# Kernel optimization log

Hardware: AMD Instinct MI355X
Metric: run time of the kernel (lower is better)

The kernel has to match this reference:

```python
import jax, jax.numpy as jnp
import numpy as np

FILTER_SIZE = 4      # pooled output size (wH = wW = 4)
STRIDE = 16          # feature stride -> spatial_scale = 1/16
C = 512              # feature_dim
H = W = 22           # feature map size (352px crop / stride 16)
NI, NS = 3, 64       # images_in_sequence, sequences
KCELLS = 6           # static bound on integer cells overlapped per bin per axis


def setup_inputs() -> dict:
    key = jax.random.key(0)
    k1, k2, k3, k4 = jax.random.split(key, 4)
    feat = jax.random.normal(k1, (NI, NS, C, H, W), dtype=jnp.float32)
    # bb = (x, y, w, h) in image coords; keep boxes inside 352px image
    xy = jax.random.uniform(k2, (NI, NS, 2), minval=0.0, maxval=96.0)
    wh = jax.random.uniform(k3, (NI, NS, 2), minval=64.0, maxval=224.0)
    bb = jnp.concatenate([xy, wh], axis=-1).astype(jnp.float32)
    # conv init: normal(0, sqrt(2/(k*k*out_ch))), zero bias (as in the torch module)
    std = np.float32(np.sqrt(2.0 / (3 * 3 * C)))
    conv_w = jax.random.normal(k4, (C, C, 3, 3), dtype=jnp.float32) * std
    conv_b = jnp.zeros((C,), jnp.float32)
    return {"feat": feat, "bb": bb, "conv_w": conv_w, "conv_b": conv_b}


def _axis_weights(start, end, size):
    """Exact PrRoIPool 1D integration weights on integer grid points.
    start, end: (N, P) continuous bin boundaries in feature coords.
    Returns (N, P, size) weights s.t. integral of the piecewise-linear
    interpolant over [start, end] = sum_i w[i] * f(i)."""
    N, P = start.shape
    s0 = jnp.floor(start).astype(jnp.int32)                  # first cell
    cell = s0[..., None] + jnp.arange(KCELLS, dtype=jnp.int32)  # (N,P,K)
    cf = cell.astype(start.dtype)
    a1 = jnp.maximum(start[..., None], cf)                   # cell-bin intersection
    a2 = jnp.maximum(jnp.minimum(end[..., None], cf + 1.0), a1)
    alpha = a1 - cf
    lim = a2 - cf
    # integral of (1-t) and t over [alpha, lim]  (PrRoIPoolingMatCalculation)
    f0 = (lim - 0.5 * lim * lim) - (alpha - 0.5 * alpha * alpha)  # weight at point `cell`
    f1 = 0.5 * lim * lim - 0.5 * alpha * alpha                    # weight at `cell+1`
    idx0, idx1 = cell, cell + 1
    v0 = (idx0 >= 0) & (idx0 < size)   # out-of-bounds feature reads are 0
    v1 = (idx1 >= 0) & (idx1 < size)
    wts = jnp.concatenate([jnp.where(v0, f0, 0.0), jnp.where(v1, f1, 0.0)], -1)
    idx = jnp.concatenate([jnp.clip(idx0, 0, size - 1), jnp.clip(idx1, 0, size - 1)], -1)
    out = jnp.zeros((N, P, size), start.dtype)
    n_i = jnp.arange(N)[:, None, None]
    p_i = jnp.arange(P)[None, :, None]
    return out.at[n_i, p_i, idx].add(wts)


def prroi_pool(feat, rois, pooled, scale):
    """Precise RoI pooling. feat: (N,C,H,W); rois: (N,4) = (x1,y1,x2,y2),
    image coords; roi i pools from image i. Returns (N,C,pooled,pooled)."""
    x1, y1, x2, y2 = (rois[:, k] * scale for k in range(4))
    bin_w = (x2 - x1) / pooled
    bin_h = (y2 - y1) / pooled
    p = jnp.arange(pooled, dtype=feat.dtype)
    sh = y1[:, None] + p * bin_h[:, None]; eh = sh + bin_h[:, None]   # (N,P)
    sw = x1[:, None] + p * bin_w[:, None]; ew = sw + bin_w[:, None]
    Wy = _axis_weights(sh, eh, feat.shape[2])   # (N,P,H)
    Wx = _axis_weights(sw, ew, feat.shape[3])   # (N,P,W)
    acc = jnp.einsum('nph,nqw,nchw->ncpq', Wy, Wx, feat)
    area = jnp.maximum(bin_h * bin_w, 0.0)[:, None, None, None]
    return jnp.where(area == 0, 0.0, acc / jnp.where(area == 0, 1.0, area))


def reference(feat, bb, conv_w, conv_b):
    ni = feat.shape[0]
    x = feat.reshape(-1, C, H, W)
    x = jax.lax.conv_general_dilated(
        x, conv_w, window_strides=(1, 1), padding=((1, 1), (1, 1)),
        dimension_numbers=('NCHW', 'OIHW', 'NCHW')) + conv_b[None, :, None, None]
    b = bb.reshape(-1, 4)
    rois = jnp.concatenate([b[:, :2], b[:, :2] + b[:, 2:]], axis=-1)  # xyxy
    w = prroi_pool(x, rois, FILTER_SIZE, 1.0 / STRIDE)
    w = w.reshape(ni, -1, C, FILTER_SIZE, FILTER_SIZE).mean(axis=0)   # mean over images
    return w / (C * FILTER_SIZE * FILTER_SIZE)                        # filter_norm
```

## Files before the change

kernel.cpp:

```cpp
#include <hip/hip_runtime.h>


#define NIMG 192
#define CCH 512
#define FH 22
#define FW 22
#define SPATIAL 484
#define KDIM 4608
#define NDIM 1024
#define KQ 8
#define KSEG 576
#define CISTRIDE 1968
#define POOLBLKS 2048

typedef __bf16 bf16;
typedef __bf16 bf16x2 __attribute__((ext_vector_type(2)));
typedef __bf16 bf16x8 __attribute__((ext_vector_type(8)));
typedef float f32x2 __attribute__((ext_vector_type(2)));
typedef float f32x4 __attribute__((ext_vector_type(4)));

#define GLOBAL_AS __attribute__((address_space(1)))
#define LDS_AS __attribute__((address_space(3)))

__device__ __forceinline__ void gload_lds16(const void* g, void* l) {
  __builtin_amdgcn_global_load_lds((GLOBAL_AS const void*)g, (LDS_AS void*)l, 16, 0, 0);
}

__device__ __forceinline__ void axis_range(float a0, float aw, int& r0, int& r1) {
  const float scale = 1.f / 16.f;
  float s1 = a0 * scale;
  float s2 = (a0 + aw) * scale;
  float bl = (s2 - s1) * 0.25f;
  float endv = (s1 + 3 * bl) + bl;
  int c0 = max(0, (int)floorf(s1));
  int c1 = min(21, (int)floorf(endv) + 1);
  r0 = max(0, c0 - 1);
  r1 = min(21, c1 + 1);
}

__device__ __forceinline__ float axis_sum(float a0, float aw, int bin) {
  const float scale = 1.f / 16.f;
  float s1 = a0 * scale;
  float s2 = (a0 + aw) * scale;
  float blen = (s2 - s1) * 0.25f;
  float start = s1 + bin * blen;
  float end = start + blen;
  float inv = 1.0f / blen;
  float S = 0.f;
  int s0i = (int)floorf(start);
  for (int kk = 0; kk < 6; ++kk) {
    int cell = s0i + kk;
    float cf = (float)cell;
    float a1 = fmaxf(start, cf);
    float a2 = fmaxf(fminf(end, cf + 1.f), a1);
    float alpha = a1 - cf, lim = a2 - cf;
    float f0 = (lim - 0.5f * lim * lim) - (alpha - 0.5f * alpha * alpha);
    float f1 = 0.5f * lim * lim - 0.5f * alpha * alpha;
    if (cell >= 0 && cell < 22) S += f0 * inv;
    if (cell + 1 >= 0 && cell + 1 < 22) S += f1 * inv;
  }
  return S;
}

__global__ __launch_bounds__(256, 4) void pool_feat_kernel(
    const float* __restrict__ feat, const float* __restrict__ bb,
    const float* __restrict__ cw, bf16* __restrict__ Wb,
    bf16* __restrict__ Gb) {
  __shared__ __align__(16) char tileb[16 * CISTRIDE];
  __shared__ float wyl3[3 * 264];
  __shared__ float wxl3[3 * 264];
  int t = threadIdx.x;
  if (blockIdx.x >= POOLBLKS) {
    int co = blockIdx.x - POOLBLKS;
    float* lw = (float*)tileb;
    const float* src = cw + (long)co * CCH * 9;
    #pragma unroll
    for (int k = 0; k < 18; ++k) lw[t + 256 * k] = src[t + 256 * k];
    __syncthreads();
    bf16* dst = Wb + (long)co * 9 * CCH;
    #pragma unroll
    for (int k = 0; k < 18; ++k) {
      int f = t + 256 * k;
      int pos = f >> 9;
      int ci = f & 511;
      dst[f] = (bf16)lw[ci * 9 + pos];
    }
    return;
  }
  int s = blockIdx.x >> 5;
  int ciq = blockIdx.x & 31;
  int p = t >> 6;
  int lane = t & 63;
  int ci16 = lane & 15;
  int vq = lane >> 4;

  f32x4 A[9];
  #pragma unroll
  for (int a = 0; a < 9; ++a) A[a] = (f32x4){0.f, 0.f, 0.f, 0.f};
  const float* tf = (const float*)tileb;

  for (int idx = t; idx < 1584; idx += 256)
    (idx < 792 ? wyl3[idx] : wxl3[idx - 792]) = 0.f;
  __syncthreads();
  if (t < 24) {
    int img = t >> 3;
    int axis = (t >> 2) & 1;
    int bin = t & 3;
    int n = img * 64 + s;
    const float scale = 1.f / 16.f;
    float a0 = axis ? bb[n * 4 + 0] : bb[n * 4 + 1];
    float aw = axis ? bb[n * 4 + 2] : bb[n * 4 + 3];
    float s1 = a0 * scale;
    float s2 = (a0 + aw) * scale;
    float blen = (s2 - s1) * 0.25f;
    float start = s1 + bin * blen;
    float end = start + blen;
    float inv = 1.0f / blen;
    float* tbl = (axis ? wxl3 : wyl3) + img * 264;
    int s0i = (int)floorf(start);
    for (int kk = 0; kk < 6; ++kk) {
      int cell = s0i + kk;
      float cf = (float)cell;
      float a1 = fmaxf(start, cf);
      float a2 = fmaxf(fminf(end, cf + 1.f), a1);
      float alpha = a1 - cf, lim = a2 - cf;
      float f0 = (lim - 0.5f * lim * lim) - (alpha - 0.5f * alpha * alpha);
      float f1 = 0.5f * lim * lim - 0.5f * alpha * alpha;
      if (cell >= 0 && cell < 22) {
        float w = f0 * inv;
        #pragma unroll
        for (int ky = 0; ky < 3; ++ky) {
          int u = cell + ky - 1;
          if (u >= 0 && u < 22) tbl[(ky * 22 + u) * 4 + bin] += w;
        }
      }
      if (cell + 1 >= 0 && cell + 1 < 22) {
        float w = f1 * inv;
        #pragma unroll
        for (int ky = 0; ky < 3; ++ky) {
          int u = cell + ky;
          if (u >= 0 && u < 22) tbl[(ky * 22 + u) * 4 + bin] += w;
        }
      }
    }
  }

  for (int img = 0; img < 3; ++img) {
    int n = img * 64 + s;
    int yr0, yr1, xr0, xr1;
    axis_range(bb[n * 4 + 1], bb[n * 4 + 3], yr0, yr1);
    axis_range(bb[n * 4 + 0], bb[n * 4 + 2], xr0, xr1);
    __syncthreads();
    int start16 = (yr0 * 88) & ~15;
    int end16 = ((yr1 + 1) * 88 + 15) & ~15;
    int cpi = (end16 - start16 + 1023) >> 10;
    const float* fpl0 = feat + ((long)n * CCH + ciq * 16) * SPATIAL;
    for (int k = p; k < 16 * cpi; k += 4) {
      int ci = (cpi == 2) ? (k >> 1) : k;
      int c = (cpi == 2) ? (k & 1) : 0;
      int cs = (c == cpi - 1) ? end16 - 1024 : start16;
      if (cs < 0) cs = 0;
      gload_lds16((const char*)(fpl0 + (long)ci * SPATIAL) + cs + lane * 16,
                  tileb + ci * CISTRIDE + cs + lane * 16);
    }
    __syncthreads();

    int vbase = xr0 & ~1;
    int npairs = ((xr1 - vbase) >> 1) + 1;
    const float* wy = wyl3 + img * 264;
    const f32x4* wx = (const f32x4*)(wxl3 + img * 264);
    const f32x2* pl2 = (const f32x2*)(tf + ci16 * (CISTRIDE / 4));

    for (int j = vq; j < npairs; j += 4) {
      int vg = vbase + 2 * j;
      float a00 = 0.f, a01 = 0.f, a10 = 0.f, a11 = 0.f, a20 = 0.f, a21 = 0.f;
      for (int u = yr0; u <= yr1; ++u) {
        f32x2 f = pl2[(u * FW + vg) >> 1];
        float w0 = wy[u * 4 + p];
        float w1 = wy[(22 + u) * 4 + p];
        float w2 = wy[(44 + u) * 4 + p];
        a00 = fmaf(w0, f[0], a00); a01 = fmaf(w0, f[1], a01);
        a10 = fmaf(w1, f[0], a10); a11 = fmaf(w1, f[1], a11);
        a20 = fmaf(w2, f[0], a20); a21 = fmaf(w2, f[1], a21);
      }
      #pragma unroll
      for (int kx = 0; kx < 3; ++kx) {
        f32x4 wx0 = wx[kx * 22 + vg];
        f32x4 wx1 = wx[kx * 22 + vg + 1];
        A[kx] += wx0 * a00 + wx1 * a01;
        A[3 + kx] += wx0 * a10 + wx1 * a11;
        A[6 + kx] += wx0 * a20 + wx1 * a21;
      }
    }
  }

  #pragma unroll
  for (int pos = 0; pos < 9; ++pos) {
    #pragma unroll
    for (int q = 0; q < 4; ++q) {
      A[pos][q] += __shfl_xor(A[pos][q], 16);
      A[pos][q] += __shfl_xor(A[pos][q], 32);
    }
  }
  if (vq == 0) {
    int ci = ciq * 16 + ci16;
    #pragma unroll
    for (int pos = 0; pos < 9; ++pos)
      #pragma unroll
      for (int q = 0; q < 4; ++q)
        Gb[(long)(s * 16 + p * 4 + q) * KDIM + pos * CCH + ci] = (bf16)A[pos][q];
  }
}

__global__ __launch_bounds__(256, 2) void gemm_kernel(const bf16* __restrict__ Wb,
                                                      const bf16* __restrict__ Gb,
                                                      float* __restrict__ Opart) {
  __shared__ __align__(16) bf16 As[128 * 64];
  __shared__ __align__(16) bf16 Bs[128 * 64];
  int bid = blockIdx.x;
  int kq = bid & 7;
  int nt = (bid >> 3) & 7;
  int mt = bid >> 6;
  int co0 = mt << 7;
  int n0 = nt << 7;
  int kbase = kq * KSEG;

  int tid = threadIdx.x;
  int wv = tid >> 6, l = tid & 63;
  int wm = wv >> 1, wn = wv & 1;
  int lrow = l >> 3;
  int cg8 = ((l & 7) ^ lrow) << 3;

  long aOff[4], bOff[4];
  #pragma unroll
  for (int j = 0; j < 4; ++j) {
    int row = j * 32 + wv * 8 + lrow;
    aOff[j] = (long)(co0 + row) * KDIM + kbase + cg8;
    bOff[j] = (long)(n0 + row) * KDIM + kbase + cg8;
  }

  const f32x4 vz = {0.f, 0.f, 0.f, 0.f};
  f32x4 acc[4][4];
  #pragma unroll
  for (int a = 0; a < 4; ++a)
    #pragma unroll
    for (int b = 0; b < 4; ++b) acc[a][b] = vz;

  for (int c = 0; c < 9; ++c) {
    long sh = c * 64;
    #pragma unroll
    for (int j = 0; j < 4; ++j) {
      gload_lds16(Wb + aOff[j] + sh, (char*)As + (j * 32 + wv * 8) * 128);
      gload_lds16(Gb + bOff[j] + sh, (char*)Bs + (j * 32 + wv * 8) * 128);
    }
    __syncthreads();
    bf16x8 af[2][4], bfv[2][4];
    #pragma unroll
    for (int kk = 0; kk < 2; ++kk) {
      #pragma unroll
      for (int i = 0; i < 4; ++i) {
        int rowa = wm * 64 + i * 16 + (l & 15);
        int offa = rowa * 128 + kk * 64 + ((l >> 4) * 16);
        offa ^= (rowa & 7) << 4;
        af[kk][i] = *(const bf16x8*)((const char*)As + offa);
        int rowb = wn * 64 + i * 16 + (l & 15);
        int offb = rowb * 128 + kk * 64 + ((l >> 4) * 16);
        offb ^= (rowb & 7) << 4;
        bfv[kk][i] = *(const bf16x8*)((const char*)Bs + offb);
      }
    }
    #pragma unroll
    for (int kk = 0; kk < 2; ++kk)
      #pragma unroll
      for (int mi = 0; mi < 4; ++mi)
        #pragma unroll
        for (int nj = 0; nj < 4; ++nj)
          acc[mi][nj] = __builtin_amdgcn_mfma_f32_16x16x32_bf16(
              af[kk][mi], bfv[kk][nj], acc[mi][nj], 0, 0, 0);
    __syncthreads();
  }

  float* op = Opart + (long)kq * CCH * NDIM;
  #pragma unroll
  for (int nj = 0; nj < 4; ++nj) {
    int nn = n0 + wn * 64 + nj * 16 + (l & 15);
    #pragma unroll
    for (int mi = 0; mi < 4; ++mi) {
      #pragma unroll
      for (int rr = 0; rr < 4; ++rr) {
        int co = co0 + wm * 64 + mi * 16 + (l >> 4) * 4 + rr;
        op[(long)co * NDIM + nn] = acc[mi][nj][rr];
      }
    }
  }
}

__global__ __launch_bounds__(256) void epi_kernel(const float* __restrict__ Opart,
                                                  const float* __restrict__ bb,
                                                  const float* __restrict__ cb,
                                                  float* __restrict__ out) {
  int t4 = blockIdx.x * 256 + threadIdx.x;
  int base = t4 * 4;
  int s = base >> 13;
  int co = (base >> 4) & 511;
  int p = (base >> 2) & 3;
  long osrc = (long)co * NDIM + s * 16 + p * 4;
  f32x4 v = *(const f32x4*)(Opart + osrc);
  #pragma unroll
  for (int kq = 1; kq < KQ; ++kq)
    v += *(const f32x4*)(Opart + (long)kq * CCH * NDIM + osrc);
  f32x4 bf4 = {0.f, 0.f, 0.f, 0.f};
  #pragma unroll
  for (int i = 0; i < 3; ++i) {
    int n = i * 64 + s;
    float Sy = axis_sum(bb[n * 4 + 1], bb[n * 4 + 3], p);
    #pragma unroll
    for (int q = 0; q < 4; ++q)
      bf4[q] += Sy * axis_sum(bb[n * 4 + 0], bb[n * 4 + 2], q);
  }
  const float fin = 1.f / (3.f * 512.f * 16.f);
  v = (v + cb[co] * bf4) * fin;
  *(f32x4*)(out + base) = v;
}

extern "C" void kernel_launch(void* const* d_in, const int* in_sizes, int n_in,
                              void* d_out, int out_size, void* d_ws, size_t ws_size,
                              hipStream_t stream) {
  const float* feat = (const float*)d_in[0];
  const float* bb = (const float*)d_in[1];
  const float* cw = (const float*)d_in[2];
  const float* cb = (const float*)d_in[3];
  float* out = (float*)d_out;

  const size_t WB_BYTES = (size_t)CCH * 9 * CCH * 2;
  const size_t GB_BYTES = (size_t)NDIM * KDIM * 2;
  const size_t OP_BYTES = (size_t)KQ * CCH * NDIM * 4;
  if (ws_size < WB_BYTES + GB_BYTES + OP_BYTES) return;

  char* ws = (char*)d_ws;
  bf16* Wb = (bf16*)ws;
  bf16* Gb = (bf16*)(ws + WB_BYTES);
  float* Opart = (float*)(ws + WB_BYTES + GB_BYTES);

  hipLaunchKernelGGL(pool_feat_kernel, dim3(POOLBLKS + CCH), dim3(256), 0, stream,
                     feat, bb, cw, Wb, Gb);
  hipLaunchKernelGGL(gemm_kernel, dim3(256), dim3(256), 0, stream, Wb, Gb, Opart);
  hipLaunchKernelGGL(epi_kernel, dim3(512), dim3(256), 0, stream, Opart, bb, cb, out);
}
```

Baseline: 71.94 us.

## Overlap pool staging with weight-table setup, shrink GEMM N tile, share epilogue bin weights

The pooling kernel now computes ROI ranges up front and issues the first image's feature load before building the weight tables. It replaces __syncthreads with explicit waitcnt barriers so the global-to-LDS copy overlaps that setup. The GEMM's N tile drops from 128 to 64, doubling the grid to 512 blocks for better CU occupancy, at the cost of more A-tile reloads. The epilogue computes the 16 bin-area factors once per block in shared memory instead of per thread.

```diff
diff --git a/kernel.cpp b/kernel.cpp
--- a/kernel.cpp
+++ b/kernel.cpp
@@ -25,6 +25,17 @@
 __device__ __forceinline__ void gload_lds16(const void* g, void* l) {
   __builtin_amdgcn_global_load_lds((GLOBAL_AS const void*)g, (LDS_AS void*)l, 16, 0, 0);
 }
+
+#define LBAR()                                                   \
+  do {                                                           \
+    asm volatile("s_waitcnt lgkmcnt(0)" ::: "memory");           \
+    __builtin_amdgcn_s_barrier();                                \
+  } while (0)
+#define FBAR()                                                   \
+  do {                                                           \
+    asm volatile("s_waitcnt vmcnt(0) lgkmcnt(0)" ::: "memory");  \
+    __builtin_amdgcn_s_barrier();                                \
+  } while (0)
 
 __device__ __forceinline__ void axis_range(float a0, float aw, int& r0, int& r1) {
   const float scale = 1.f / 16.f;
@@ -94,14 +105,69 @@
   int ci16 = lane & 15;
   int vq = lane >> 4;
 
+  int yr0a[3], yr1a[3], xr0a[3], xr1a[3];
+  #pragma unroll
+  for (int i = 0; i < 3; ++i) {
+    int n = i * 64 + s;
+    axis_range(bb[n * 4 + 1], bb[n * 4 + 3], yr0a[i], yr1a[i]);
+    axis_range(bb[n * 4 + 0], bb[n * 4 + 2], xr0a[i], xr1a[i]);
+  }
+
   f32x4 A[9];
   #pragma unroll
   for (int a = 0; a < 9; ++a) A[a] = (f32x4){0.f, 0.f, 0.f, 0.f};
   const float* tf = (const float*)tileb;
 
+  auto STAGE = [&](int img) {
+    int n = img * 64 + s;
+    int start16 = (yr0a[img] * 88) & ~15;
+    int end16 = ((yr1a[img] + 1) * 88 + 15) & ~15;
+    int cpi = (end16 - start16 + 1023) >> 10;
+    const float* fpl0 = feat + ((long)n * CCH + ciq * 16) * SPATIAL;
+    for (int k = p; k < 16 * cpi; k += 4) {
+      int ci = (cpi == 2) ? (k >> 1) : k;
+      int c = (cpi == 2) ? (k & 1) : 0;
+      int cs = (c == cpi - 1) ? end16 - 1024 : start16;
+      if (cs < 0) cs = 0;
+      gload_lds16((const char*)(fpl0 + (long)ci * SPATIAL) + cs + lane * 16,
+                  tileb + ci * CISTRIDE + cs + lane * 16);
+    }
+  };
+
+  auto COMPUTE = [&](int img) {
+    int yr0 = yr0a[img], yr1 = yr1a[img];
+    int vbase = xr0a[img] & ~1;
+    int npairs = ((xr1a[img] - vbase) >> 1) + 1;
+    const float* wy = wyl3 + img * 264;
+    const f32x4* wx = (const f32x4*)(wxl3 + img * 264);
+    const f32x2* pl2 = (const f32x2*)(tf + ci16 * (CISTRIDE / 4));
+    for (int j = vq; j < npairs; j += 4) {
+      int vg = vbase + 2 * j;
+      float a00 = 0.f, a01 = 0.f, a10 = 0.f, a11 = 0.f, a20 = 0.f, a21 = 0.f;
+      for (int u = yr0; u <= yr1; ++u) {
+        f32x2 f = pl2[(u * FW + vg) >> 1];
+        float w0 = wy[u * 4 + p];
+        float w1 = wy[(22 + u) * 4 + p];
+        float w2 = wy[(44 + u) * 4 + p];
+        a00 = fmaf(w0, f[0], a00); a01 = fmaf(w0, f[1], a01);
+        a10 = fmaf(w1, f[0], a10); a11 = fmaf(w1, f[1], a11);
+        a20 = fmaf(w2, f[0], a20); a21 = fmaf(w2, f[1], a21);
+      }
+      #pragma unroll
+      for (int kx = 0; kx < 3; ++kx) {
+        f32x4 wx0 = wx[kx * 22 + vg];
+        f32x4 wx1 = wx[kx * 22 + vg + 1];
+        A[kx] += wx0 * a00 + wx1 * a01;
+        A[3 + kx] += wx0 * a10 + wx1 * a11;
+        A[6 + kx] += wx0 * a20 + wx1 * a21;
+      }
+    }
+  };
+
+  STAGE(0);
   for (int idx = t; idx < 1584; idx += 256)
     (idx < 792 ? wyl3[idx] : wxl3[idx - 792]) = 0.f;
-  __syncthreads();
+  LBAR();
   if (t < 24) {
     int img = t >> 3;
     int axis = (t >> 2) & 1;
@@ -144,54 +210,14 @@
       }
     }
   }
-
-  for (int img = 0; img < 3; ++img) {
-    int n = img * 64 + s;
-    int yr0, yr1, xr0, xr1;
-    axis_range(bb[n * 4 + 1], bb[n * 4 + 3], yr0, yr1);
-    axis_range(bb[n * 4 + 0], bb[n * 4 + 2], xr0, xr1);
-    __syncthreads();
-    int start16 = (yr0 * 88) & ~15;
-    int end16 = ((yr1 + 1) * 88 + 15) & ~15;
-    int cpi = (end16 - start16 + 1023) >> 10;
-    const float* fpl0 = feat + ((long)n * CCH + ciq * 16) * SPATIAL;
-    for (int k = p; k < 16 * cpi; k += 4) {
-      int ci = (cpi == 2) ? (k >> 1) : k;
-      int c = (cpi == 2) ? (k & 1) : 0;
-      int cs = (c == cpi - 1) ? end16 - 1024 : start16;
-      if (cs < 0) cs = 0;
-      gload_lds16((const char*)(fpl0 + (long)ci * SPATIAL) + cs + lane * 16,
-                  tileb + ci * CISTRIDE + cs + lane * 16);
-    }
-    __syncthreads();
-
-    int vbase = xr0 & ~1;
-    int npairs = ((xr1 - vbase) >> 1) + 1;
-    const float* wy = wyl3 + img * 264;
-    const f32x4* wx = (const f32x4*)(wxl3 + img * 264);
-    const f32x2* pl2 = (const f32x2*)(tf + ci16 * (CISTRIDE / 4));
-
-    for (int j = vq; j < npairs; j += 4) {
-      int vg = vbase + 2 * j;
-      float a00 = 0.f, a01 = 0.f, a10 = 0.f, a11 = 0.f, a20 = 0.f, a21 = 0.f;
-      for (int u = yr0; u <= yr1; ++u) {
-        f32x2 f = pl2[(u * FW + vg) >> 1];
-        float w0 = wy[u * 4 + p];
-        float w1 = wy[(22 + u) * 4 + p];
-        float w2 = wy[(44 + u) * 4 + p];
-        a00 = fmaf(w0, f[0], a00); a01 = fmaf(w0, f[1], a01);
-        a10 = fmaf(w1, f[0], a10); a11 = fmaf(w1, f[1], a11);
-        a20 = fmaf(w2, f[0], a20); a21 = fmaf(w2, f[1], a21);
-      }
-      #pragma unroll
-      for (int kx = 0; kx < 3; ++kx) {
-        f32x4 wx0 = wx[kx * 22 + vg];
-        f32x4 wx1 = wx[kx * 22 + vg + 1];
-        A[kx] += wx0 * a00 + wx1 * a01;
-        A[3 + kx] += wx0 * a10 + wx1 * a11;
-        A[6 + kx] += wx0 * a20 + wx1 * a21;
-      }
-    }
+  FBAR();
+  COMPUTE(0);
+  #pragma unroll 1
+  for (int img = 1; img < 3; ++img) {
+    LBAR();
+    STAGE(img);
+    FBAR();
+    COMPUTE(img);
   }
 
   #pragma unroll
@@ -216,13 +242,13 @@
                                                       const bf16* __restrict__ Gb,
                                                       float* __restrict__ Opart) {
   __shared__ __align__(16) bf16 As[128 * 64];
-  __shared__ __align__(16) bf16 Bs[128 * 64];
+  __shared__ __align__(16) bf16 Bs[64 * 64];
   int bid = blockIdx.x;
   int kq = bid & 7;
-  int nt = (bid >> 3) & 7;
-  int mt = bid >> 6;
+  int nt = (bid >> 3) & 15;
+  int mt = bid >> 7;
   int co0 = mt << 7;
-  int n0 = nt << 7;
+  int n0 = nt << 6;
   int kbase = kq * KSEG;
 
   int tid = threadIdx.x;
@@ -231,30 +257,35 @@
   int lrow = l >> 3;
   int cg8 = ((l & 7) ^ lrow) << 3;
 
-  long aOff[4], bOff[4];
+  long aOff[4], bOff[2];
   #pragma unroll
   for (int j = 0; j < 4; ++j) {
     int row = j * 32 + wv * 8 + lrow;
     aOff[j] = (long)(co0 + row) * KDIM + kbase + cg8;
+  }
+  #pragma unroll
+  for (int j = 0; j < 2; ++j) {
+    int row = j * 32 + wv * 8 + lrow;
     bOff[j] = (long)(n0 + row) * KDIM + kbase + cg8;
   }
 
   const f32x4 vz = {0.f, 0.f, 0.f, 0.f};
-  f32x4 acc[4][4];
+  f32x4 acc[4][2];
   #pragma unroll
   for (int a = 0; a < 4; ++a)
     #pragma unroll
-    for (int b = 0; b < 4; ++b) acc[a][b] = vz;
+    for (int b = 0; b < 2; ++b) acc[a][b] = vz;
 
   for (int c = 0; c < 9; ++c) {
     long sh = c * 64;
     #pragma unroll
-    for (int j = 0; j < 4; ++j) {
+    for (int j = 0; j < 4; ++j)
       gload_lds16(Wb + aOff[j] + sh, (char*)As + (j * 32 + wv * 8) * 128);
+    #pragma unroll
+    for (int j = 0; j < 2; ++j)
       gload_lds16(Gb + bOff[j] + sh, (char*)Bs + (j * 32 + wv * 8) * 128);
-    }
     __syncthreads();
-    bf16x8 af[2][4], bfv[2][4];
+    bf16x8 af[2][4], bfv[2][2];
     #pragma unroll
     for (int kk = 0; kk < 2; ++kk) {
       #pragma unroll
@@ -263,7 +294,10 @@
         int offa = rowa * 128 + kk * 64 + ((l >> 4) * 16);
         offa ^= (rowa & 7) << 4;
         af[kk][i] = *(const bf16x8*)((const char*)As + offa);
-        int rowb = wn * 64 + i * 16 + (l & 15);
+      }
+      #pragma unroll
+      for (int i = 0; i < 2; ++i) {
+        int rowb = wn * 32 + i * 16 + (l & 15);
         int offb = rowb * 128 + kk * 64 + ((l >> 4) * 16);
         offb ^= (rowb & 7) << 4;
         bfv[kk][i] = *(const bf16x8*)((const char*)Bs + offb);
@@ -274,7 +308,7 @@
       #pragma unroll
       for (int mi = 0; mi < 4; ++mi)
         #pragma unroll
-        for (int nj = 0; nj < 4; ++nj)
+        for (int nj = 0; nj < 2; ++nj)
           acc[mi][nj] = __builtin_amdgcn_mfma_f32_16x16x32_bf16(
               af[kk][mi], bfv[kk][nj], acc[mi][nj], 0, 0, 0);
     __syncthreads();
@@ -282,8 +316,8 @@
 
   float* op = Opart + (long)kq * CCH * NDIM;
   #pragma unroll
-  for (int nj = 0; nj < 4; ++nj) {
-    int nn = n0 + wn * 64 + nj * 16 + (l & 15);
+  for (int nj = 0; nj < 2; ++nj) {
+    int nn = n0 + wn * 32 + nj * 16 + (l & 15);
     #pragma unroll
     for (int mi = 0; mi < 4; ++mi) {
       #pragma unroll
@@ -299,9 +333,24 @@
                                                   const float* __restrict__ bb,
                                                   const float* __restrict__ cb,
                                                   float* __restrict__ out) {
-  int t4 = blockIdx.x * 256 + threadIdx.x;
-  int base = t4 * 4;
-  int s = base >> 13;
+  __shared__ float bfl[16];
+  int bid = blockIdx.x;
+  int t = threadIdx.x;
+  int s = bid >> 3;
+  if (t < 16) {
+    int p = t >> 2;
+    int q = t & 3;
+    float acc = 0.f;
+    #pragma unroll
+    for (int i = 0; i < 3; ++i) {
+      int n = i * 64 + s;
+      acc += axis_sum(bb[n * 4 + 1], bb[n * 4 + 3], p) *
+             axis_sum(bb[n * 4 + 0], bb[n * 4 + 2], q);
+    }
+    bfl[t] = acc;
+  }
+  __syncthreads();
+  int base = (bid * 256 + t) * 4;
   int co = (base >> 4) & 511;
   int p = (base >> 2) & 3;
   long osrc = (long)co * NDIM + s * 16 + p * 4;
@@ -309,15 +358,7 @@
   #pragma unroll
   for (int kq = 1; kq < KQ; ++kq)
     v += *(const f32x4*)(Opart + (long)kq * CCH * NDIM + osrc);
-  f32x4 bf4 = {0.f, 0.f, 0.f, 0.f};
-  #pragma unroll
-  for (int i = 0; i < 3; ++i) {
-    int n = i * 64 + s;
-    float Sy = axis_sum(bb[n * 4 + 1], bb[n * 4 + 3], p);
-    #pragma unroll
-    for (int q = 0; q < 4; ++q)
-      bf4[q] += Sy * axis_sum(bb[n * 4 + 0], bb[n * 4 + 2], q);
-  }
+  f32x4 bf4 = {bfl[p * 4 + 0], bfl[p * 4 + 1], bfl[p * 4 + 2], bfl[p * 4 + 3]};
   const float fin = 1.f / (3.f * 512.f * 16.f);
   v = (v + cb[co] * bf4) * fin;
   *(f32x4*)(out + base) = v;
@@ -344,6 +385,6 @@
 
   hipLaunchKernelGGL(pool_feat_kernel, dim3(POOLBLKS + CCH), dim3(256), 0, stream,
                      feat, bb, cw, Wb, Gb);
-  hipLaunchKernelGGL(gemm_kernel, dim3(256), dim3(256), 0, stream, Wb, Gb, Opart);
+  hipLaunchKernelGGL(gemm_kernel, dim3(512), dim3(256), 0, stream, Wb, Gb, Opart);
   hipLaunchKernelGGL(epi_kernel, dim3(512), dim3(256), 0, stream, Opart, bb, cb, out);
 }
```

Result: faster. 69.78 us (-3.0%).
